# Performance work log

Measured on AMD Instinct MI355X. Metric: run time of the kernel, lower is better.

Reference implementation:

```python
import jax, jax.numpy as jnp
import numpy as np
import math

NEG = -1e30  # sentinel for suppressed scores
MAX_OUT = 2000  # nms_index[:2000]
NMS_THR = 0.7


def conv2d(x, w, b, padding):
    y = jax.lax.conv_general_dilated(x, w, (1, 1), padding,
                                     dimension_numbers=('NCHW', 'OIHW', 'NCHW'))
    return y + b[None, :, None, None]


def make_anchors(img_h, img_w, gh, gw):
    # Faithful to RPN.make_anchor_box: centers at (i+0.5)*stride; note the
    # torch meshgrid/reshape quirk makes xy[a,b] = (cx[a], cy[b]) for square grids.
    assert gh == gw
    areas = [128.0 ** 2, 256.0 ** 2, 512.0 ** 2]
    ratios = [(1.0, 1.0), (2.0, 1.0), (1.0, 2.0)]
    cx = (np.arange(gw) + 0.5) * (img_w / gw)
    cy = (np.arange(gh) + 0.5) * (img_h / gh)
    X = np.broadcast_to(cx[:, None], (gh, gw))
    Y = np.broadcast_to(cy[None, :], (gh, gw))
    anchs = []
    for area in areas:
        for wr, hr in ratios:
            u = math.sqrt(area / (wr * hr))
            w, h = wr * u, hr * u
            anchs.append(np.stack([X - w / 2, Y - h / 2, X + w / 2, Y + h / 2], axis=-1))
    A = np.stack(anchs, axis=2).reshape(-1, 4).astype(np.float32)  # [gh*gw*9, 4]
    return jnp.asarray(A)


def iou_one_vs_all(box, boxes):
    x1 = jnp.maximum(box[0], boxes[:, 0]); y1 = jnp.maximum(box[1], boxes[:, 1])
    x2 = jnp.minimum(box[2], boxes[:, 2]); y2 = jnp.minimum(box[3], boxes[:, 3])
    inter = jnp.clip(x2 - x1, 0.0) * jnp.clip(y2 - y1, 0.0)
    a1 = (box[2] - box[0]) * (box[3] - box[1])
    a2 = (boxes[:, 2] - boxes[:, 0]) * (boxes[:, 3] - boxes[:, 1])
    return inter / (a1 + a2 - inter + 1e-9)


def greedy_nms(boxes, scores):
    # sequential greedy NMS, MAX_OUT picks; suppressed slots carry score NEG
    def step(s, _):
        j = jnp.argmax(s)
        ok = s[j] > NEG * 0.5
        iou = iou_one_vs_all(boxes[j], boxes)
        s = jnp.where(iou > NMS_THR, NEG, s).at[j].set(NEG)
        return s, (j, ok)
    _, (idxs, valid) = jax.lax.scan(step, scores, None, length=MAX_OUT)
    return idxs, valid


def rpn_forward(x, conv_w, conv_b, bbox_w, bbox_b, score_w, score_b, img_h, img_w):
    gh, gw = x.shape[-2], x.shape[-1]
    h = jax.nn.relu(conv2d(x, conv_w, conv_b, 'SAME'))
    # note: both heads pass through ReLU in the original Sequentials
    breg = jax.nn.relu(conv2d(h, bbox_w, bbox_b, 'VALID')).reshape(-1, 4)  # (C,H,W) flatten, as torch .view
    obj = jax.nn.relu(conv2d(h, score_w, score_b, 'VALID')).reshape(-1, 2)
    anchors = make_anchors(img_h, img_w, gh, gw)
    # box decode
    wa = anchors[:, 2] - anchors[:, 0]; ha = anchors[:, 3] - anchors[:, 1]
    cxa = (anchors[:, 0] + anchors[:, 2]) * 0.5; cya = (anchors[:, 1] + anchors[:, 3]) * 0.5
    cx = breg[:, 0] * wa + cxa; cy = breg[:, 1] * ha + cya
    w = jnp.exp(breg[:, 2]) * wa; hh = jnp.exp(breg[:, 3]) * ha
    boxes = jnp.stack([cx - w / 2, cy - hh / 2, cx + w / 2, cy + hh / 2], axis=1)
    # proposal_filter: clip to image (N = 9*gh*gw < 200000, so topk branch is skipped)
    boxes = jnp.stack([
        jnp.clip(boxes[:, 0], 0.0, float(img_w)),
        jnp.clip(boxes[:, 1], 0.0, float(img_h)),
        jnp.clip(boxes[:, 2], 0.0, float(img_w)),
        jnp.clip(boxes[:, 3], 0.0, float(img_h))], axis=1)
    score0 = obj[:, 0]
    area = jnp.abs((boxes[:, 0] - boxes[:, 2]) * (boxes[:, 1] - boxes[:, 3]))
    keep = (score0 > 0.2) & (area > 100.0)
    s = jnp.where(keep, score0, NEG)
    idxs, valid = greedy_nms(jax.lax.stop_gradient(boxes), jax.lax.stop_gradient(s))
    out_boxes = jnp.where(valid[:, None], boxes[idxs], 0.0)   # [2000,4], zero-padded
    out_scores = jnp.where(valid[:, None], obj[idxs], 0.0)    # [2000,2]
    return out_boxes, out_scores


def setup_inputs() -> dict:
    key = jax.random.key(0)
    ks = jax.random.split(key, 5)
    in_ch, gh, gw = 256, 96, 96
    x = jax.random.normal(ks[0], (1, in_ch, gh, gw), jnp.float32)
    conv_w = jax.random.normal(ks[1], (in_ch, in_ch, 3, 3), jnp.float32) / math.sqrt(in_ch * 9)
    conv_b = jnp.zeros((in_ch,), jnp.float32)
    bbox_w = jax.random.normal(ks[2], (36, in_ch, 1, 1), jnp.float32) / math.sqrt(in_ch)
    bbox_b = jnp.zeros((36,), jnp.float32)
    score_w = jax.random.normal(ks[3], (18, in_ch, 1, 1), jnp.float32) / math.sqrt(in_ch)
    score_b = jnp.zeros((18,), jnp.float32)
    return {"x": x, "conv_w": conv_w, "conv_b": conv_b, "bbox_w": bbox_w,
            "bbox_b": bbox_b, "score_w": score_w, "score_b": score_b,
            "img_h": 1536, "img_w": 1536}


def reference(x, conv_w, conv_b, bbox_w, bbox_b, score_w, score_b, img_h, img_w):
    return rpn_forward(x, conv_w, conv_b, bbox_w, bbox_b, score_w, score_b, img_h, img_w)
```

## Files before the change

kernel.cpp:

```cpp
#include <hip/hip_runtime.h>
#include <hip/hip_bf16.h>
#include <math.h>

#define SGRID 9216
#define NANCH 82944
#define NSORT 131072
#define TOPM  8192
#define MAXOUT 2000
#define OCB 32
#define XPS 104
#define XCS (98 * XPS)

__device__ __forceinline__ bool iou_gt07(const float4 bi, const float4 bj) {
  float a1 = __fmul_rn(bi.z - bi.x, bi.w - bi.y);
  float a2 = __fmul_rn(bj.z - bj.x, bj.w - bj.y);
  float xx1 = fmaxf(bi.x, bj.x), yy1 = fmaxf(bi.y, bj.y);
  float xx2 = fminf(bi.z, bj.z), yy2 = fminf(bi.w, bj.w);
  float inter = __fmul_rn(fmaxf(xx2 - xx1, 0.f), fmaxf(yy2 - yy1, 0.f));
  float den = ((a1 + a2) - inter) + 1e-9f;
  return __fdiv_rn(inter, den) > 0.7f;
}

__global__ void k_init(unsigned long long* keys, unsigned int* ctrs) {
  int i = blockIdx.x * 256 + threadIdx.x;
  if (i < NSORT) keys[i] = 0ull;
  if (i < 8) ctrs[i] = 0u;
}

__global__ void k_pad(const float* __restrict__ x, float* __restrict__ xpad) {
  for (size_t i = (size_t)blockIdx.x * 256 + threadIdx.x; i < (size_t)256 * XCS;
       i += (size_t)gridDim.x * 256) {
    int ic = (int)(i / XCS);
    int rem = (int)(i % XCS);
    int yy = rem / XPS, xx = rem % XPS;
    float v = 0.f;
    if (yy >= 1 && yy <= 96 && xx >= 1 && xx <= 96)
      v = x[(size_t)ic * SGRID + (yy - 1) * 96 + (xx - 1)];
    xpad[i] = v;
  }
}

__global__ void k_wre(const float* __restrict__ w, float* __restrict__ wre) {
  for (size_t i = (size_t)blockIdx.x * 256 + threadIdx.x; i < (size_t)32 * 256 * 72;
       i += (size_t)gridDim.x * 256) {
    int c = (int)(i / (256 * 72));
    int rem = (int)(i % (256 * 72));
    int oc = rem / 72, j = rem % 72;
    wre[i] = w[(size_t)oc * 2304 + c * 72 + j];
  }
}

__global__ __launch_bounds__(256) void k_conv3(const float* __restrict__ xpad,
                                               const float* __restrict__ wre,
                                               const float* __restrict__ bias,
                                               float* __restrict__ h) {
  __shared__ float xsB[2][8][320];
  __shared__ float wB[2][2304];
  const int y = blockIdx.x;
  const int oc0 = blockIdx.y * OCB;
  const int t = threadIdx.x;
  const int og = t >> 4;
  const int xg = t & 15;
  float acc[2][6];
#pragma unroll
  for (int a = 0; a < 2; a++)
#pragma unroll
    for (int c = 0; c < 6; c++) acc[a][c] = 0.f;

  int xg_ofs[3], xl_ofs[3];
  bool xon[3];
#pragma unroll
  for (int k = 0; k < 3; k++) {
    int idx = t + k * 256;
    xon[k] = (idx < 624);
    int rowidx = idx / 26, col = idx - rowidx * 26;
    int ic = rowidx / 3, r = rowidx - ic * 3;
    if (!xon[k]) { ic = 0; r = 0; col = 0; }
    xg_ofs[k] = ic * XCS + (y + r) * XPS + col * 4;
    xl_ofs[k] = ic * 320 + r * XPS + col * 4;
  }
  int won[3];
#pragma unroll
  for (int k = 0; k < 3; k++) won[k] = ((t + k * 256) < 576);

  float4 xv[3], wv[3];
  auto ldreg = [&](int c) {
    const float* xb = xpad + (size_t)c * 8 * XCS;
    const float* wb = wre + ((size_t)c * 256 + oc0) * 72;
#pragma unroll
    for (int k = 0; k < 3; k++)
      if (xon[k]) xv[k] = *(const float4*)(xb + xg_ofs[k]);
#pragma unroll
    for (int k = 0; k < 3; k++)
      if (won[k]) wv[k] = *(const float4*)(wb + (t + k * 256) * 4);
  };
  auto stlds = [&](int buf) {
    float* xd = &xsB[buf][0][0];
#pragma unroll
    for (int k = 0; k < 3; k++)
      if (xon[k]) *(float4*)(xd + xl_ofs[k]) = xv[k];
#pragma unroll
    for (int k = 0; k < 3; k++)
      if (won[k]) *(float4*)(&wB[buf][(t + k * 256) * 4]) = wv[k];
  };

  ldreg(0);
  stlds(0);
  ldreg(1);
  __syncthreads();
  int buf = 0;
  for (int c = 0; c < 32; c++) {
    if (c < 31) {
      stlds(buf ^ 1);
      if (c < 30) ldreg(c + 2);
    }
#pragma unroll
    for (int ic = 0; ic < 8; ic++) {
#pragma unroll
      for (int r = 0; r < 3; r++) {
        float xr[8];
#pragma unroll
        for (int u = 0; u < 8; u++) xr[u] = xsB[buf][ic][r * XPS + xg * 6 + u];
#pragma unroll
        for (int a = 0; a < 2; a++) {
          float w0 = wB[buf][(og * 2 + a) * 72 + ic * 9 + r * 3 + 0];
          float w1 = wB[buf][(og * 2 + a) * 72 + ic * 9 + r * 3 + 1];
          float w2 = wB[buf][(og * 2 + a) * 72 + ic * 9 + r * 3 + 2];
#pragma unroll
          for (int c2 = 0; c2 < 6; c2++)
            acc[a][c2] += xr[c2] * w0 + xr[c2 + 1] * w1 + xr[c2 + 2] * w2;
        }
      }
    }
    __syncthreads();
    buf ^= 1;
  }
#pragma unroll
  for (int a = 0; a < 2; a++) {
    int oc = oc0 + og * 2 + a;
    float bb = bias[oc];
#pragma unroll
    for (int c = 0; c < 6; c++) {
      float v = acc[a][c] + bb;
      h[(size_t)oc * SGRID + y * 96 + xg * 6 + c] = v > 0.f ? v : 0.f;
    }
  }
}

__global__ __launch_bounds__(256) void k_conv1x1(const float* __restrict__ h,
                                                 const float* __restrict__ bw, const float* __restrict__ bb,
                                                 const float* __restrict__ sw, const float* __restrict__ sb,
                                                 float* __restrict__ bbox, float* __restrict__ score) {
  __shared__ float wcat[54][256];
  const int t = threadIdx.x;
  for (int idx = t; idx < 54 * 64; idx += 256) {
    int c = idx >> 6, k4 = idx & 63;
    const float* src = (c < 36) ? (bw + c * 256) : (sw + (c - 36) * 256);
    float4 v = *(const float4*)(src + k4 * 4);
    *(float4*)(&wcat[c][k4 * 4]) = v;
  }
  __syncthreads();
  const int p = blockIdx.x * 256 + t;
  float accA[54];
#pragma unroll
  for (int c = 0; c < 54; c++) accA[c] = 0.f;
  for (int k0 = 0; k0 < 256; k0 += 8) {
    float ha[8];
#pragma unroll
    for (int u = 0; u < 8; u++) ha[u] = h[(size_t)(k0 + u) * SGRID + p];
#pragma unroll
    for (int c = 0; c < 54; c++) {
      float4 w0 = *(const float4*)(&wcat[c][k0]);
      float4 w1 = *(const float4*)(&wcat[c][k0 + 4]);
      accA[c] += ha[0] * w0.x + ha[1] * w0.y + ha[2] * w0.z + ha[3] * w0.w
               + ha[4] * w1.x + ha[5] * w1.y + ha[6] * w1.z + ha[7] * w1.w;
    }
  }
#pragma unroll
  for (int c = 0; c < 36; c++) {
    float va = accA[c] + bb[c];
    bbox[(size_t)c * SGRID + p] = va > 0.f ? va : 0.f;
  }
#pragma unroll
  for (int c = 36; c < 54; c++) {
    float va = accA[c] + sb[c - 36];
    score[(size_t)(c - 36) * SGRID + p] = va > 0.f ? va : 0.f;
  }
}

__global__ void k_decode(const float* __restrict__ bbox, const float* __restrict__ score,
                         float4* __restrict__ boxes, unsigned long long* __restrict__ keys,
                         unsigned int* __restrict__ cnt) {
  int a = blockIdx.x * 256 + threadIdx.x;
  if (a >= NANCH) return;
  int i = a / 864;
  int rem = a - i * 864;
  int j = rem / 9;
  int k = rem - j * 9;
  const double areas[3] = {16384.0, 65536.0, 262144.0};
  int ai = k / 3, ri = k - ai * 3;
  double wr = (ri == 1) ? 2.0 : 1.0;
  double hr = (ri == 2) ? 2.0 : 1.0;
  double u = sqrt(areas[ai] / (wr * hr));
  double wd = wr * u, hd = hr * u;
  double cxd = (i + 0.5) * 16.0, cyd = (j + 0.5) * 16.0;
  float ax1 = (float)(cxd - wd * 0.5), ax2 = (float)(cxd + wd * 0.5);
  float ay1 = (float)(cyd - hd * 0.5), ay2 = (float)(cyd + hd * 0.5);
  float wa = ax2 - ax1, haa = ay2 - ay1;
  float cxa = (ax1 + ax2) * 0.5f, cya = (ay1 + ay2) * 0.5f;

  float4 br = ((const float4*)bbox)[a];
  float o0 = score[2 * (size_t)a];

  float cx = __fmul_rn(br.x, wa) + cxa;
  float cy = __fmul_rn(br.y, haa) + cya;
  float ww = __fmul_rn(expf(br.z), wa);
  float hh = __fmul_rn(expf(br.w), haa);
  float x1 = fminf(fmaxf(cx - __fmul_rn(ww, 0.5f), 0.f), 1536.f);
  float y1 = fminf(fmaxf(cy - __fmul_rn(hh, 0.5f), 0.f), 1536.f);
  float x2 = fminf(fmaxf(cx + __fmul_rn(ww, 0.5f), 0.f), 1536.f);
  float y2 = fminf(fmaxf(cy + __fmul_rn(hh, 0.5f), 0.f), 1536.f);
  boxes[a] = make_float4(x1, y1, x2, y2);
  float area = fabsf(__fmul_rn(x1 - x2, y1 - y2));
  if (o0 > 0.2f && area > 100.0f) {
    unsigned p = atomicAdd(cnt, 1u);
    keys[p] = ((unsigned long long)__float_as_uint(o0) << 32) |
              (unsigned long long)(0xFFFFFFFFu - (unsigned)a);
  }
}

__global__ __launch_bounds__(1024) void k_sort_local(unsigned long long* keys) {
  __shared__ unsigned long long s[4096];
  const int base = blockIdx.x * 4096, t = threadIdx.x;
  for (int u = t; u < 4096; u += 1024) s[u] = keys[base + u];
  __syncthreads();
  for (int k = 2; k <= 4096; k <<= 1) {
    for (int j = k >> 1; j >= 1; j >>= 1) {
      for (int m = t; m < 2048; m += 1024) {
        int i = ((m & ~(j - 1)) << 1) | (m & (j - 1));
        int l = i | j;
        bool dir = (((base + i) & k) == 0);
        unsigned long long A = s[i], B = s[l];
        bool sw = dir ? (A < B) : (A > B);
        if (sw) { s[i] = B; s[l] = A; }
      }
      __syncthreads();
    }
  }
  for (int u = t; u < 4096; u += 1024) keys[base + u] = s[u];
}

__global__ void k_sort_global(unsigned long long* keys, int k, int j) {
  int m = blockIdx.x * 256 + threadIdx.x;
  int i = ((m & ~(j - 1)) << 1) | (m & (j - 1));
  int l = i | j;
  bool dir = ((i & k) == 0);
  unsigned long long A = keys[i], B = keys[l];
  bool sw = dir ? (A < B) : (A > B);
  if (sw) { keys[i] = B; keys[l] = A; }
}

__global__ __launch_bounds__(1024) void k_sort_localmerge(unsigned long long* keys, int k) {
  __shared__ unsigned long long s[4096];
  const int base = blockIdx.x * 4096, t = threadIdx.x;
  for (int u = t; u < 4096; u += 1024) s[u] = keys[base + u];
  __syncthreads();
  const bool dir = ((base & k) == 0);
  for (int j = 2048; j >= 1; j >>= 1) {
    for (int m = t; m < 2048; m += 1024) {
      int i = ((m & ~(j - 1)) << 1) | (m & (j - 1));
      int l = i | j;
      unsigned long long A = s[i], B = s[l];
      bool sw = dir ? (A < B) : (A > B);
      if (sw) { s[i] = B; s[l] = A; }
    }
    __syncthreads();
  }
  for (int u = t; u < 4096; u += 1024) keys[base + u] = s[u];
}

__global__ void k_gather(const unsigned long long* __restrict__ keys,
                         const float4* __restrict__ boxes,
                         float4* __restrict__ sbox, unsigned int* __restrict__ sidx,
                         const unsigned int* __restrict__ cntp) {
  int p = blockIdx.x * 256 + threadIdx.x;
  if (p >= TOPM) return;
  unsigned c = *cntp;
  if (p < (int)c) {
    unsigned a = 0xFFFFFFFFu - (unsigned)(keys[p] & 0xFFFFFFFFull);
    sbox[p] = boxes[a];
    sidx[p] = a;
  } else {
    sbox[p] = make_float4(3e9f, 3e9f, 3e9f, 3e9f);
    sidx[p] = 0u;
  }
}

__global__ __launch_bounds__(256) void k_mask(const float4* __restrict__ sbox,
                                              unsigned long long* __restrict__ mask) {
  if ((int)(blockIdx.y * 8 + 7) < (int)blockIdx.x) return;
  __shared__ float4 jb[512];
  const int i0 = blockIdx.x * 64;
  const int j0 = blockIdx.y * 512;
  const int t = threadIdx.x;
  for (int u = t; u < 512; u += 256) jb[u] = sbox[j0 + u];
  __syncthreads();
  const int il = t & 63, grp = t >> 6;
  const int i = i0 + il;
  const float4 bi = sbox[i];
#pragma unroll
  for (int wwi = 0; wwi < 2; wwi++) {
    int w = grp * 2 + wwi;
    unsigned long long bits = 0ull;
    for (int b = 0; b < 64; b++) {
      if (iou_gt07(bi, jb[w * 64 + b])) bits |= (1ull << b);
    }
    mask[(size_t)i * (TOPM / 64) + (j0 >> 6) + w] = bits;
  }
}

__global__ __launch_bounds__(1024) void k_sweepA(const unsigned int* __restrict__ sidx,
                                                 const unsigned long long* __restrict__ mask,
                                                 unsigned int* __restrict__ ctrs,
                                                 unsigned int* __restrict__ acc) {
  __shared__ unsigned long long removed[TOPM / 64];
  __shared__ unsigned long long selfm[2][64];
  __shared__ unsigned int sidxw[2][64];
  __shared__ unsigned char saccb[64];
  __shared__ unsigned int snacc, sna;
  const int t = threadIdx.x;
  const unsigned cnt = ctrs[0];
  const unsigned M = cnt < TOPM ? cnt : TOPM;
  const unsigned nwords = (M + 63u) >> 6;
  if (t < TOPM / 64) removed[t] = 0ull;
  if (t == 0) { sna = 0u; snacc = 0u; }
  if (nwords > 0 && t < 64) {
    selfm[0][t] = mask[(size_t)t * (TOPM / 64) + 0];
    sidxw[0][t] = sidx[t];
  }
  __syncthreads();
  for (unsigned wi = 0; wi < nwords; wi++) {
    const int cur = (int)(wi & 1u);
    if (t == 0) {
      unsigned rem0 = M - wi * 64u;
      unsigned long long valid = (rem0 >= 64u) ? ~0ull : ((1ull << rem0) - 1ull);
      unsigned long long w = ~removed[wi] & valid;
      unsigned nacc = 0u, na_l = sna;
      while (w && na_l < MAXOUT) {
        int b = __builtin_ctzll(w);
        saccb[nacc++] = (unsigned char)b;
        acc[na_l++] = sidxw[cur][b];
        w &= ~selfm[cur][b];
        w &= ~(1ull << b);
      }
      snacc = nacc;
      sna = na_l;
    }
    __syncthreads();
    if (wi + 1u < nwords && t < 64) {
      selfm[cur ^ 1][t] = mask[(size_t)((wi + 1u) * 64u + t) * (TOPM / 64) + (wi + 1u)];
      sidxw[cur ^ 1][t] = sidx[(wi + 1u) * 64u + t];
    }
    {
      const unsigned nacc = snacc;
      const int wj = t & 127, g = t >> 7;
      if (nacc && (unsigned)g < nacc && wj > (int)wi) {
        unsigned long long a0 = 0ull, a1 = 0ull;
        unsigned k2 = (unsigned)g;
        for (; k2 + 8u < nacc; k2 += 16u) {
          a0 |= mask[(size_t)(wi * 64u + saccb[k2]) * (TOPM / 64) + wj];
          a1 |= mask[(size_t)(wi * 64u + saccb[k2 + 8u]) * (TOPM / 64) + wj];
        }
        for (; k2 < nacc; k2 += 8u)
          a0 |= mask[(size_t)(wi * 64u + saccb[k2]) * (TOPM / 64) + wj];
        unsigned long long accum = a0 | a1;
        if (accum) atomicOr(&removed[wj], accum);
      }
    }
    __syncthreads();
    if (sna >= MAXOUT) break;
  }
  if (t == 0) ctrs[1] = sna;
}

__global__ void k_abox(const float4* __restrict__ boxes, const unsigned int* __restrict__ acc,
                       const unsigned int* __restrict__ ctrs, float4* __restrict__ abox) {
  unsigned i = blockIdx.x * 256 + threadIdx.x;
  if (i < ctrs[1]) abox[i] = boxes[acc[i]];
}

__global__ __launch_bounds__(256) void k_filter(const unsigned long long* __restrict__ keys,
                                                const float4* __restrict__ boxes,
                                                const unsigned int* __restrict__ ctrs,
                                                const float4* __restrict__ abox,
                                                unsigned char* __restrict__ flags) {
  __shared__ float4 at[256];
  const int t = threadIdx.x;
  const unsigned cnt = ctrs[0], naA = ctrs[1];
  if (naA >= MAXOUT) return;
  const unsigned q = TOPM + blockIdx.x * 256 + t;
  float4 bq = make_float4(3e9f, 3e9f, 3e9f, 3e9f);
  unsigned flag = 0u;
  if (q < cnt) {
    unsigned a = 0xFFFFFFFFu - (unsigned)(keys[q] & 0xFFFFFFFFull);
    bq = boxes[a];
    flag = 1u;
  }
  for (unsigned u0 = 0; u0 < naA; u0 += 256u) {
    unsigned m = naA - u0; if (m > 256u) m = 256u;
    if ((unsigned)t < m) at[t] = abox[u0 + t];
    __syncthreads();
    if (flag) {
      for (unsigned u = 0; u < m; u++)
        if (iou_gt07(at[u], bq)) { flag = 0u; break; }
    }
    __syncthreads();
  }
  if (q < cnt) flags[q - TOPM] = (unsigned char)flag;
}

__global__ __launch_bounds__(1024) void k_compact(const unsigned long long* __restrict__ keys,
                                                  unsigned int* __restrict__ ctrs,
                                                  const unsigned char* __restrict__ flags,
                                                  unsigned int* __restrict__ said) {
  __shared__ unsigned wsum[16], wpre[16];
  __shared__ unsigned base, tot;
  const int t = threadIdx.x, wid = t >> 6, lane = t & 63;
  const unsigned cnt = ctrs[0], naA = ctrs[1];
  if (naA >= MAXOUT || cnt <= TOPM) { if (t == 0) ctrs[2] = 0u; return; }
  const unsigned n = cnt - TOPM;
  if (t == 0) base = 0u;
  __syncthreads();
  for (unsigned s = 0; s < n; s += 1024u) {
    unsigned q = s + t;
    bool pred = (q < n) && flags[q];
    unsigned long long ball = __ballot(pred);
    if (lane == 0) wsum[wid] = (unsigned)__popcll(ball);
    __syncthreads();
    if (t == 0) {
      unsigned a2 = 0;
      for (int i = 0; i < 16; i++) { wpre[i] = a2; a2 += wsum[i]; }
      tot = a2;
    }
    __syncthreads();
    if (pred) {
      unsigned pos = base + wpre[wid] +
                     (unsigned)__popcll(ball & ((lane == 0) ? 0ull : ((1ull << lane) - 1ull)));
      said[pos] = 0xFFFFFFFFu - (unsigned)(keys[TOPM + q] & 0xFFFFFFFFull);
    }
    __syncthreads();
    if (t == 0) base += tot;
    __syncthreads();
  }
  if (t == 0) ctrs[2] = base;
}

__global__ __launch_bounds__(256) void k_nmsB(const unsigned int* __restrict__ said,
                                              const float4* __restrict__ boxes,
                                              unsigned int* __restrict__ ctrs,
                                              unsigned int* __restrict__ acc) {
  __shared__ float4 ab[MAXOUT];
  __shared__ float4 cb[64];
  __shared__ unsigned int cba[64];
  __shared__ unsigned long long selfm[64];
  __shared__ unsigned long long ssup;
  __shared__ unsigned int sna;
  const int t = threadIdx.x;
  const unsigned naA = ctrs[1], scnt = ctrs[2];
  if (naA >= MAXOUT || scnt == 0u) return;
  if (t == 0) sna = 0u;
  __syncthreads();
  for (unsigned q0 = 0; q0 < scnt; q0 += 64) {
    unsigned nr = scnt - q0; if (nr > 64u) nr = 64u;
    if (t < 64) {
      if ((unsigned)t < nr) {
        unsigned a = said[q0 + t];
        cba[t] = a;
        cb[t] = boxes[a];
      } else {
        cb[t] = make_float4(3e9f, 3e9f, 3e9f, 3e9f);
        cba[t] = 0u;
      }
    }
    if (t == 0) ssup = 0ull;
    __syncthreads();
    if (t < 64) {
      float4 bi = cb[t];
      unsigned long long bits = 0ull;
      for (int b = 0; b < 64; b++)
        if (iou_gt07(bi, cb[b])) bits |= (1ull << b);
      selfm[t] = bits;
    }
    const unsigned na0 = sna;
    unsigned long long mybits = 0ull;
    const int colg = (t & 3) * 16;
    for (unsigned u = (unsigned)(t >> 2); u < na0; u += 64u) {
      float4 au = ab[u];
#pragma unroll
      for (int b2 = 0; b2 < 16; b2++)
        if (iou_gt07(au, cb[colg + b2])) mybits |= (1ull << (colg + b2));
    }
    if (mybits) atomicOr(&ssup, mybits);
    __syncthreads();
    if (t == 0) {
      unsigned long long w = ~ssup;
      if (nr < 64u) w &= ((1ull << nr) - 1ull);
      unsigned na = sna;
      while (w && (naA + na) < MAXOUT) {
        int b = __builtin_ctzll(w);
        ab[na] = cb[b];
        acc[naA + na] = cba[b];
        na++;
        w &= ~selfm[b];
      }
      sna = na;
    }
    __syncthreads();
    if (naA + sna >= MAXOUT) break;
  }
  if (t == 0) ctrs[1] = naA + sna;
}

__global__ void k_output(const float4* __restrict__ boxes, const float* __restrict__ score,
                         const unsigned int* __restrict__ acc, const unsigned int* __restrict__ ctrs,
                         float* __restrict__ out) {
  int tdx = blockIdx.x * 256 + threadIdx.x;
  if (tdx >= MAXOUT) return;
  unsigned na = ctrs[1];
  float4 b = make_float4(0.f, 0.f, 0.f, 0.f);
  float o0 = 0.f, o1 = 0.f;
  if (tdx < (int)na) {
    unsigned a = acc[tdx];
    b = boxes[a];
    o0 = score[2 * (size_t)a];
    o1 = score[2 * (size_t)a + 1];
  }
  out[tdx * 4 + 0] = b.x;
  out[tdx * 4 + 1] = b.y;
  out[tdx * 4 + 2] = b.z;
  out[tdx * 4 + 3] = b.w;
  out[8000 + tdx * 2 + 0] = o0;
  out[8000 + tdx * 2 + 1] = o1;
}

__global__ __launch_bounds__(256) void k_probe(const float* __restrict__ h,
                                               const float* __restrict__ score,
                                               const unsigned long long* __restrict__ keys,
                                               const unsigned int* __restrict__ ctrs,
                                               float* __restrict__ out) {
  __shared__ unsigned sf;
  const int t = threadIdx.x;
  if (t == 0) sf = 0u;
  __syncthreads();
  unsigned local = 0u;
  for (int i = t; i < 4096; i += 256)
    if (h[(size_t)i * 575] > 0.f) { local |= 1u; break; }
  for (int i = t; i < 4096; i += 256)
    if (score[(size_t)i * 40] > 0.2f) { local |= 2u; break; }
  if (t == 0) {
    unsigned cnt = ctrs[0], na = ctrs[1];
    if (cnt > 0u)                local |= 4u;
    if (cnt >= 4096u)            local |= 8u;
    if ((keys[0] >> 32) != 0ull) local |= 16u;
    if (na >= 1u)                local |= 32u;
  }
  atomicOr(&sf, local);
  __syncthreads();
  if (t == 0 && (sf & 63u) != 63u) out[0] = 1e6f * (1.f + (float)sf);
}

extern "C" void kernel_launch(void* const* d_in, const int* in_sizes, int n_in,
                              void* d_out, int out_size, void* d_ws, size_t ws_size,
                              hipStream_t stream) {
  const float* x       = (const float*)d_in[0];
  const float* conv_w  = (const float*)d_in[1];
  const float* conv_b  = (const float*)d_in[2];
  const float* bbox_w  = (const float*)d_in[3];
  const float* bbox_b  = (const float*)d_in[4];
  const float* score_w = (const float*)d_in[5];
  const float* score_b = (const float*)d_in[6];

  char* ws = (char*)d_ws;
  size_t off = 0;
  auto alloc = [&](size_t bytes) {
    void* p = ws + off;
    off = (off + bytes + 255) & ~(size_t)255;
    return p;
  };
  float* h = (float*)alloc((size_t)256 * SGRID * 4);
  char*  R = (char*)alloc((size_t)13292544 + 512);
  float* xpad = (float*)R;
  float* wre  = (float*)(R + 10446848);
  float* bbox              = (float*)(R + 0);
  float* score             = (float*)(R + 1327104);
  float4* boxes            = (float4*)(R + 1990656);
  unsigned long long* keys = (unsigned long long*)(R + 3317760);
  float4* sbox             = (float4*)(R + 4366336);
  unsigned int* sidx       = (unsigned int*)(R + 4497408);
  unsigned long long* mask = (unsigned long long*)(R + 4530176);
  unsigned char* flags     = (unsigned char*)(R + 12918784);
  unsigned int* said       = (unsigned int*)(R + 12993536);
  unsigned int* acc        = (unsigned int*)alloc((size_t)2048 * 4);
  float4* abox             = (float4*)alloc((size_t)2048 * 16);
  unsigned int* ctrs       = (unsigned int*)alloc(64);
  unsigned int* cnt = ctrs + 0;
  (void)in_sizes; (void)n_in; (void)out_size; (void)ws_size;

  k_pad<<<2048, 256, 0, stream>>>(x, xpad);
  k_wre<<<1024, 256, 0, stream>>>(conv_w, wre);
  k_conv3<<<dim3(96, 256 / OCB), 256, 0, stream>>>(xpad, wre, conv_b, h);

  k_init<<<NSORT / 256, 256, 0, stream>>>(keys, ctrs);
  k_conv1x1<<<36, 256, 0, stream>>>(h, bbox_w, bbox_b, score_w, score_b, bbox, score);
  k_decode<<<NANCH / 256, 256, 0, stream>>>(bbox, score, boxes, keys, cnt);

  k_sort_local<<<NSORT / 4096, 1024, 0, stream>>>(keys);
  for (int k = 8192; k <= NSORT; k <<= 1) {
    for (int j = k >> 1; j >= 4096; j >>= 1)
      k_sort_global<<<NSORT / 512, 256, 0, stream>>>(keys, k, j);
    k_sort_localmerge<<<NSORT / 4096, 1024, 0, stream>>>(keys, k);
  }

  k_gather<<<TOPM / 256, 256, 0, stream>>>(keys, boxes, sbox, sidx, cnt);
  k_mask<<<dim3(TOPM / 64, TOPM / 512), 256, 0, stream>>>(sbox, mask);
  k_sweepA<<<1, 1024, 0, stream>>>(sidx, mask, ctrs, acc);
  k_abox<<<8, 256, 0, stream>>>(boxes, acc, ctrs, abox);

  k_filter<<<(NANCH - TOPM + 255) / 256, 256, 0, stream>>>(keys, boxes, ctrs, abox, flags);
  k_compact<<<1, 1024, 0, stream>>>(keys, ctrs, flags, said);
  k_nmsB<<<1, 256, 0, stream>>>(said, boxes, ctrs, acc);

  k_output<<<(MAXOUT + 255) / 256, 256, 0, stream>>>(boxes, score, acc, ctrs, (float*)d_out);
  k_probe<<<1, 256, 0, stream>>>(h, score, keys, ctrs, (float*)d_out);
}
```

Before: 863.7 us.

## Split conv3 rows in halves with transposed weight layout and 128-thread blocks

The 3x3 convolution now splits each output row into two halves of 48 columns, using 128-thread blocks over a (96,2,8) grid, which doubles the block count. The weights are re-laid out so the output channel is innermost, and threads are remapped so lanes walk output channels, making the weight reads from shared memory contiguous. This raises occupancy and aims to cut LDS bank conflicts. In exchange, the input halo is loaded twice across the halves and per-block work shrinks.

```diff
diff --git a/kernel.cpp b/kernel.cpp
--- a/kernel.cpp
+++ b/kernel.cpp
@@ -40,27 +40,31 @@
   }
 }
 
-__global__ void k_wre(const float* __restrict__ w, float* __restrict__ wre) {
-  for (size_t i = (size_t)blockIdx.x * 256 + threadIdx.x; i < (size_t)32 * 256 * 72;
+__global__ void k_wre2(const float* __restrict__ w, float* __restrict__ wre2) {
+  for (size_t i = (size_t)blockIdx.x * 256 + threadIdx.x; i < (size_t)32 * 8 * 72 * 32;
        i += (size_t)gridDim.x * 256) {
-    int c = (int)(i / (256 * 72));
-    int rem = (int)(i % (256 * 72));
-    int oc = rem / 72, j = rem % 72;
-    wre[i] = w[(size_t)oc * 2304 + c * 72 + j];
-  }
-}
-
-__global__ __launch_bounds__(256) void k_conv3(const float* __restrict__ xpad,
-                                               const float* __restrict__ wre,
+    int c = (int)(i / 18432);
+    int rem = (int)(i % 18432);
+    int b = rem / 2304;
+    int rem2 = rem % 2304;
+    int j = rem2 / 32, oc = rem2 % 32;
+    wre2[i] = w[(size_t)(b * 32 + oc) * 2304 + c * 72 + j];
+  }
+}
+
+__global__ __launch_bounds__(128) void k_conv3(const float* __restrict__ xpad,
+                                               const float* __restrict__ wre2,
                                                const float* __restrict__ bias,
                                                float* __restrict__ h) {
-  __shared__ float xsB[2][8][320];
-  __shared__ float wB[2][2304];
+  __shared__ float xsB[2][8 * 3 * 56];
+  __shared__ float wB[2][72 * 32];
   const int y = blockIdx.x;
-  const int oc0 = blockIdx.y * OCB;
+  const int half = blockIdx.y;
+  const int h0 = half * 44;
+  const int hofs = half * 4;
   const int t = threadIdx.x;
-  const int og = t >> 4;
-  const int xg = t & 15;
+  const int og = t & 15;
+  const int xg = t >> 4;
   float acc[2][6];
 #pragma unroll
   for (int a = 0; a < 2; a++)
@@ -71,37 +75,37 @@
   bool xon[3];
 #pragma unroll
   for (int k = 0; k < 3; k++) {
-    int idx = t + k * 256;
-    xon[k] = (idx < 624);
-    int rowidx = idx / 26, col = idx - rowidx * 26;
-    int ic = rowidx / 3, r = rowidx - ic * 3;
-    if (!xon[k]) { ic = 0; r = 0; col = 0; }
-    xg_ofs[k] = ic * XCS + (y + r) * XPS + col * 4;
-    xl_ofs[k] = ic * 320 + r * XPS + col * 4;
-  }
-  int won[3];
-#pragma unroll
-  for (int k = 0; k < 3; k++) won[k] = ((t + k * 256) < 576);
-
-  float4 xv[3], wv[3];
+    int idx = t + k * 128;
+    xon[k] = (idx < 336);
+    int ic = idx / 42, rem = idx - ic * 42;
+    int r = rem / 14, q = rem - r * 14;
+    if (!xon[k]) { ic = 0; r = 0; q = 0; }
+    xg_ofs[k] = ic * XCS + (y + r) * XPS + h0 + q * 4;
+    xl_ofs[k] = ic * 168 + r * 56 + q * 4;
+  }
+  bool won[5];
+#pragma unroll
+  for (int k = 0; k < 5; k++) won[k] = ((t + k * 128) < 576);
+
+  float4 xv[3], wv[5];
   auto ldreg = [&](int c) {
     const float* xb = xpad + (size_t)c * 8 * XCS;
-    const float* wb = wre + ((size_t)c * 256 + oc0) * 72;
+    const float* wb = wre2 + ((size_t)c * 8 + blockIdx.z) * 2304;
 #pragma unroll
     for (int k = 0; k < 3; k++)
       if (xon[k]) xv[k] = *(const float4*)(xb + xg_ofs[k]);
 #pragma unroll
-    for (int k = 0; k < 3; k++)
-      if (won[k]) wv[k] = *(const float4*)(wb + (t + k * 256) * 4);
+    for (int k = 0; k < 5; k++)
+      if (won[k]) wv[k] = *(const float4*)(wb + (t + k * 128) * 4);
   };
   auto stlds = [&](int buf) {
-    float* xd = &xsB[buf][0][0];
+    float* xd = xsB[buf];
 #pragma unroll
     for (int k = 0; k < 3; k++)
       if (xon[k]) *(float4*)(xd + xl_ofs[k]) = xv[k];
 #pragma unroll
-    for (int k = 0; k < 3; k++)
-      if (won[k]) *(float4*)(&wB[buf][(t + k * 256) * 4]) = wv[k];
+    for (int k = 0; k < 5; k++)
+      if (won[k]) *(float4*)(&wB[buf][(t + k * 128) * 4]) = wv[k];
   };
 
   ldreg(0);
@@ -119,13 +123,15 @@
 #pragma unroll
       for (int r = 0; r < 3; r++) {
         float xr[8];
-#pragma unroll
-        for (int u = 0; u < 8; u++) xr[u] = xsB[buf][ic][r * XPS + xg * 6 + u];
+        const float* xrow = &xsB[buf][ic * 168 + r * 56 + hofs + xg * 6];
+#pragma unroll
+        for (int u = 0; u < 8; u++) xr[u] = xrow[u];
+        const int j0 = (ic * 9 + r * 3) * 32 + og * 2;
 #pragma unroll
         for (int a = 0; a < 2; a++) {
-          float w0 = wB[buf][(og * 2 + a) * 72 + ic * 9 + r * 3 + 0];
-          float w1 = wB[buf][(og * 2 + a) * 72 + ic * 9 + r * 3 + 1];
-          float w2 = wB[buf][(og * 2 + a) * 72 + ic * 9 + r * 3 + 2];
+          float w0 = wB[buf][j0 + a];
+          float w1 = wB[buf][j0 + 32 + a];
+          float w2 = wB[buf][j0 + 64 + a];
 #pragma unroll
           for (int c2 = 0; c2 < 6; c2++)
             acc[a][c2] += xr[c2] * w0 + xr[c2 + 1] * w1 + xr[c2 + 2] * w2;
@@ -137,12 +143,12 @@
   }
 #pragma unroll
   for (int a = 0; a < 2; a++) {
-    int oc = oc0 + og * 2 + a;
+    int oc = blockIdx.z * OCB + og * 2 + a;
     float bb = bias[oc];
 #pragma unroll
     for (int c = 0; c < 6; c++) {
       float v = acc[a][c] + bb;
-      h[(size_t)oc * SGRID + y * 96 + xg * 6 + c] = v > 0.f ? v : 0.f;
+      h[(size_t)oc * SGRID + y * 96 + half * 48 + xg * 6 + c] = v > 0.f ? v : 0.f;
     }
   }
 }
@@ -590,7 +596,7 @@
   float* h = (float*)alloc((size_t)256 * SGRID * 4);
   char*  R = (char*)alloc((size_t)13292544 + 512);
   float* xpad = (float*)R;
-  float* wre  = (float*)(R + 10446848);
+  float* wre2 = (float*)(R + 10446848);
   float* bbox              = (float*)(R + 0);
   float* score             = (float*)(R + 1327104);
   float4* boxes            = (float4*)(R + 1990656);
@@ -607,8 +613,8 @@
   (void)in_sizes; (void)n_in; (void)out_size; (void)ws_size;
 
   k_pad<<<2048, 256, 0, stream>>>(x, xpad);
-  k_wre<<<1024, 256, 0, stream>>>(conv_w, wre);
-  k_conv3<<<dim3(96, 256 / OCB), 256, 0, stream>>>(xpad, wre, conv_b, h);
+  k_wre2<<<1024, 256, 0, stream>>>(conv_w, wre2);
+  k_conv3<<<dim3(96, 2, 8), 128, 0, stream>>>(xpad, wre2, conv_b, h);
 
   k_init<<<NSORT / 256, 256, 0, stream>>>(keys, ctrs);
   k_conv1x1<<<36, 256, 0, stream>>>(h, bbox_w, bbox_b, score_w, score_b, bbox, score);
```

Measured after the change: 916.1 us. 6.1% more time.
